# Optimization experiments

Hardware: AMD Instinct MI355X
Metric: run time of the kernel (lower is better)

The kernel has to match this reference:

```python
import jax, jax.numpy as jnp
import numpy as np

N = 300000   # number of occupied voxels (sparse tensor rows)
L = 100      # grid side length -> 1e6 cells, occupancy 0.3
C = 32       # channels (channelwise/depthwise conv)
KS = 3       # kernel_size per axis
D = 3        # spatial dimension
R = (KS - 1) // 2


def _build_sparse_structure():
    """Sample N unique voxel coords and build kernel maps (edge lists) like
    MinkowskiEngine's coordinate manager: for each kernel offset, pairs
    (in_idx, out_idx) such that coords[in_idx] == coords[out_idx] + offset."""
    rng = np.random.default_rng(0)
    flat = rng.choice(L ** 3, size=N, replace=False)
    coords = np.stack([flat // (L * L), (flat // L) % L, flat % L], axis=1).astype(np.int32)
    keys = flat.astype(np.int64)
    order = np.argsort(keys)
    sk = keys[order]
    out_ids = np.arange(N, dtype=np.int64)
    in_list, out_list = [], []
    for dx in range(-R, R + 1):
        for dy in range(-R, R + 1):
            for dz in range(-R, R + 1):
                nx = coords[:, 0].astype(np.int64) + dx
                ny = coords[:, 1].astype(np.int64) + dy
                nz = coords[:, 2].astype(np.int64) + dz
                inb = (nx >= 0) & (nx < L) & (ny >= 0) & (ny < L) & (nz >= 0) & (nz < L)
                nk = (nx * L + ny) * L + nz
                pos = np.searchsorted(sk, nk)
                pos_c = np.clip(pos, 0, N - 1)
                ok = inb & (sk[pos_c] == nk)
                in_list.append(order[pos_c[ok]])
                out_list.append(out_ids[ok])
    in_idx = np.concatenate(in_list).astype(np.int32)
    out_idx = np.concatenate(out_list).astype(np.int32)
    return coords, in_idx, out_idx


def setup_inputs() -> dict:
    coords, in_idx, out_idx = _build_sparse_structure()
    key = jax.random.key(0)
    k1, k2 = jax.random.split(key)
    in_feats = jax.random.normal(k1, (N, C), dtype=jnp.float32)
    kernel = jax.random.normal(k2, (KS ** D, C), dtype=jnp.float32)  # depthwise kernel
    return {
        "coords": jnp.asarray(coords),
        "in_idx": jnp.asarray(in_idx),
        "out_idx": jnp.asarray(out_idx),
        "in_feats": in_feats,
        "kernel": kernel,
    }


def reference(coords, in_idx, out_idx, in_feats, kernel):
    # index_array = KS ** flip(arange(D)) -> [9, 3, 1] for KS=3, D=3
    index_pow = jnp.array([KS ** (D - 1 - i) for i in range(D)], dtype=jnp.int32)
    # tensor_stride = 1; kernel_coord = (C_in - C_out)//1 + (KS-1)//2, per edge [E, D]
    kernel_coord = coords[in_idx] - coords[out_idx] + R
    k1d = jnp.sum(index_pow[None, :] * kernel_coord, axis=1)  # [E] in [0, KS**D)
    # gather-multiply-scatter: out_F[out] += in_feats[in] * kernel[k1d]
    out_F = jnp.zeros_like(in_feats).at[out_idx].add(in_feats[in_idx] * kernel[k1d])
    return out_F
```

## Files before the change

### kernel.cpp

```cpp
#include <hip/hip_runtime.h>

#define NCH 32
#define GROUPS 8
#define KVOL 27
#define LG 100
#define LP 102
#define RGN 5
#define NRGN 20
#define NREGIONS (NRGN * NRGN * NRGN)
#define BSIDE 7
#define BVOL 343
#define CELLS 125
#define LSTR 29

__global__ void build_dense(const int* __restrict__ coords,
                            int* __restrict__ dense, int N) {
    int i = blockIdx.x * blockDim.x + threadIdx.x;
    if (i >= N) return;
    int x = coords[3 * i + 0];
    int y = coords[3 * i + 1];
    int z = coords[3 * i + 2];
    dense[((size_t)(x + 1) * LP + (y + 1)) * LP + (z + 1)] = i + 1;
}

__global__ __launch_bounds__(256) void gather_conv_region(
        const int* __restrict__ dense,
        const float4* __restrict__ in_feats4,
        const float4* __restrict__ kernel4,
        float4* __restrict__ out4) {
    __shared__ float4 kw[(KVOL + 1) * GROUPS];
    __shared__ int brick[BVOL];
    __shared__ int rows[CELLS];
    __shared__ int cnts[CELLS];
    __shared__ int list[CELLS * LSTR];
    __shared__ int cnt;

    int tid = threadIdx.x;

    int b = blockIdx.x;
    const int per = NREGIONS >> 3;
    int r = (b & 7) * per + (b >> 3);

    if (tid == 0) cnt = 0;
    for (int i = tid; i < (KVOL + 1) * GROUPS; i += 256)
        kw[i] = (i < KVOL * GROUPS) ? kernel4[i]
                                    : make_float4(0.f, 0.f, 0.f, 0.f);

    int bx = r / (NRGN * NRGN);
    int by = (r / NRGN) % NRGN;
    int bz = r % NRGN;
    int ox = bx * RGN, oy = by * RGN, oz = bz * RGN;

    for (int i = tid; i < BVOL; i += 256) {
        int lx = i / (BSIDE * BSIDE), ly = (i / BSIDE) % BSIDE, lz = i % BSIDE;
        brick[i] = dense[((size_t)(ox + lx) * LP + (oy + ly)) * LP + (oz + lz)];
    }
    __syncthreads();

    if (tid < CELLS) {
        int cx = tid / (RGN * RGN), cy = (tid / RGN) % RGN, cz = tid % RGN;
        int bidx = (cx + 1) * (BSIDE * BSIDE) + (cy + 1) * BSIDE + (cz + 1);
        int v = brick[bidx];
        if (v > 0) {
            int p = atomicAdd(&cnt, 1);
            int myrow = v - 1;
            rows[p] = myrow;
            int j = 0;
            #pragma unroll
            for (int k = 0; k < KVOL; ++k) {
                int dx = k / 9 - 1, dy = (k / 3) % 3 - 1, dz = k % 3 - 1;
                int nb = brick[bidx + dx * (BSIDE * BSIDE) + dy * BSIDE + dz];
                if (nb > 0) list[p * LSTR + (j++)] = ((nb - 1) << 5) | k;
            }
            while (j & 3) list[p * LSTR + (j++)] = (myrow << 5) | KVOL;
            cnts[p] = j;
        }
    }
    __syncthreads();

    int n  = cnt;
    int lr = tid >> 3;
    int g  = tid & 7;
    for (int base = 0; base < n; base += 32) {
        int lo = base + lr;
        if (lo < n) {
            int cr = cnts[lo];
            const int* tl = &list[lo * LSTR];
            float4 acc = make_float4(0.f, 0.f, 0.f, 0.f);
            for (int j = 0; j < cr; j += 4) {
                int e0 = tl[j + 0], e1 = tl[j + 1];
                int e2 = tl[j + 2], e3 = tl[j + 3];
                float4 f0 = in_feats4[(size_t)(e0 >> 5) * GROUPS + g];
                float4 f1 = in_feats4[(size_t)(e1 >> 5) * GROUPS + g];
                float4 f2 = in_feats4[(size_t)(e2 >> 5) * GROUPS + g];
                float4 f3 = in_feats4[(size_t)(e3 >> 5) * GROUPS + g];
                float4 w0 = kw[(e0 & 31) * GROUPS + g];
                float4 w1 = kw[(e1 & 31) * GROUPS + g];
                float4 w2 = kw[(e2 & 31) * GROUPS + g];
                float4 w3 = kw[(e3 & 31) * GROUPS + g];
                acc.x += f0.x * w0.x; acc.y += f0.y * w0.y;
                acc.z += f0.z * w0.z; acc.w += f0.w * w0.w;
                acc.x += f1.x * w1.x; acc.y += f1.y * w1.y;
                acc.z += f1.z * w1.z; acc.w += f1.w * w1.w;
                acc.x += f2.x * w2.x; acc.y += f2.y * w2.y;
                acc.z += f2.z * w2.z; acc.w += f2.w * w2.w;
                acc.x += f3.x * w3.x; acc.y += f3.y * w3.y;
                acc.z += f3.z * w3.z; acc.w += f3.w * w3.w;
            }
            out4[(size_t)rows[lo] * GROUPS + g] = acc;
        }
    }
}

__global__ void mink_conv_scatter(const int* __restrict__ coords,
                                  const int* __restrict__ in_idx,
                                  const int* __restrict__ out_idx,
                                  const float4* __restrict__ in_feats4,
                                  const float4* __restrict__ kernel4,
                                  float* __restrict__ out,
                                  int E) {
    __shared__ float4 kw[KVOL * GROUPS];
    for (int i = threadIdx.x; i < KVOL * GROUPS; i += blockDim.x)
        kw[i] = kernel4[i];
    __syncthreads();
    int t = blockIdx.x * blockDim.x + threadIdx.x;
    if (t >= E * GROUPS) return;
    int e = t >> 3, g = t & 7;
    int vi = in_idx[e], vo = out_idx[e];
    int c0 = coords[vi * 3 + 0] - coords[vo * 3 + 0] + 1;
    int c1 = coords[vi * 3 + 1] - coords[vo * 3 + 1] + 1;
    int c2 = coords[vi * 3 + 2] - coords[vo * 3 + 2] + 1;
    int k1d = (c0 * 3 + c1) * 3 + c2;
    float4 f = in_feats4[vi * GROUPS + g];
    float4 w = kw[k1d * GROUPS + g];
    float* o = out + vo * NCH + g * 4;
    atomicAdd(o + 0, f.x * w.x);
    atomicAdd(o + 1, f.y * w.y);
    atomicAdd(o + 2, f.z * w.z);
    atomicAdd(o + 3, f.w * w.w);
}

extern "C" void kernel_launch(void* const* d_in, const int* in_sizes, int n_in,
                              void* d_out, int out_size, void* d_ws, size_t ws_size,
                              hipStream_t stream) {
    const int*   coords   = (const int*)d_in[0];
    const int*   in_idx   = (const int*)d_in[1];
    const int*   out_idx  = (const int*)d_in[2];
    const float* in_feats = (const float*)d_in[3];
    const float* kernel   = (const float*)d_in[4];

    const int E     = in_sizes[1];
    const int Nrows = out_size / NCH;

    const size_t dense_bytes = (size_t)LP * LP * LP * sizeof(int);

    if (ws_size >= dense_bytes) {
        int* dense = (int*)d_ws;
        hipMemsetAsync(dense, 0, dense_bytes, stream);

        int block = 256;
        int grid1 = (Nrows + block - 1) / block;
        build_dense<<<grid1, block, 0, stream>>>(coords, dense, Nrows);

        gather_conv_region<<<NREGIONS, 256, 0, stream>>>(
            dense, (const float4*)in_feats, (const float4*)kernel,
            (float4*)d_out);
    } else {
        hipMemsetAsync(d_out, 0, (size_t)out_size * sizeof(float), stream);
        int total = E * GROUPS;
        int block = 256;
        int grid  = (total + block - 1) / block;
        mink_conv_scatter<<<grid, block, 0, stream>>>(
            coords, in_idx, out_idx,
            (const float4*)in_feats, (const float4*)kernel,
            (float*)d_out, E);
    }
}
```

Measured before the change: 144.6 us.

## Stage brick neighbor features in LDS and pack edge lists as 16-bit slot indices

Each region block now assigns LDS slots to all occupied voxels of its 7x7x7 brick, halo included, and loads their features into shared memory once. Edge lists then hold 16-bit slot|offset codes instead of global rows. This removes repeated global gathers of the same neighbor feature rows across the 27 offsets. List building runs on 64 threads while the other threads fill the feature staging buffer, and LDS arrays use a padded stride of 9 float4 per row to reduce bank conflicts. If a brick has more than 167 occupied voxels, a fallback path gathers features from global memory. The larger LDS footprint may lower occupancy.

```diff
diff --git a/kernel.cpp b/kernel.cpp
--- a/kernel.cpp
+++ b/kernel.cpp
@@ -11,7 +11,10 @@
 #define BSIDE 7
 #define BVOL 343
 #define CELLS 125
-#define LSTR 29
+#define FSTRIDE 9
+#define FEAT_SLOTS 168
+#define FEAT_CAP (FEAT_SLOTS - 1)
+#define LSTR 28
 
 __global__ void build_dense(const int* __restrict__ coords,
                             int* __restrict__ dense, int N) {
@@ -28,23 +31,28 @@
         const float4* __restrict__ in_feats4,
         const float4* __restrict__ kernel4,
         float4* __restrict__ out4) {
-    __shared__ float4 kw[(KVOL + 1) * GROUPS];
-    __shared__ int brick[BVOL];
-    __shared__ int rows[CELLS];
-    __shared__ int cnts[CELLS];
-    __shared__ int list[CELLS * LSTR];
-    __shared__ int cnt;
+    __shared__ float4 feat[FEAT_SLOTS * FSTRIDE];
+    __shared__ float4 kw[(KVOL + 1) * FSTRIDE];
+    __shared__ int bs[BVOL];
+    __shared__ int slotrow[BVOL + 1];
+    __shared__ int cellq[CELLS];
+    __shared__ __align__(16) unsigned short list[CELLS * LSTR];
+    __shared__ int nslots, nint;
 
     int tid = threadIdx.x;
+    int g   = tid & 7;
+
+    if (tid == 0) { nslots = 0; nint = 0; slotrow[0] = 0; }
+    if (tid < (KVOL + 1) * GROUPS) {
+        int kr = tid >> 3;
+        kw[kr * FSTRIDE + g] = (kr < KVOL) ? kernel4[kr * GROUPS + g]
+                                           : make_float4(0.f, 0.f, 0.f, 0.f);
+    }
+    if (tid < GROUPS) feat[tid] = make_float4(0.f, 0.f, 0.f, 0.f);
 
     int b = blockIdx.x;
     const int per = NREGIONS >> 3;
     int r = (b & 7) * per + (b >> 3);
-
-    if (tid == 0) cnt = 0;
-    for (int i = tid; i < (KVOL + 1) * GROUPS; i += 256)
-        kw[i] = (i < KVOL * GROUPS) ? kernel4[i]
-                                    : make_float4(0.f, 0.f, 0.f, 0.f);
 
     int bx = r / (NRGN * NRGN);
     int by = (r / NRGN) % NRGN;
@@ -53,61 +61,113 @@
 
     for (int i = tid; i < BVOL; i += 256) {
         int lx = i / (BSIDE * BSIDE), ly = (i / BSIDE) % BSIDE, lz = i % BSIDE;
-        brick[i] = dense[((size_t)(ox + lx) * LP + (oy + ly)) * LP + (oz + lz)];
-    }
-    __syncthreads();
-
-    if (tid < CELLS) {
-        int cx = tid / (RGN * RGN), cy = (tid / RGN) % RGN, cz = tid % RGN;
-        int bidx = (cx + 1) * (BSIDE * BSIDE) + (cy + 1) * BSIDE + (cz + 1);
-        int v = brick[bidx];
+        bs[i] = dense[((size_t)(ox + lx) * LP + (oy + ly)) * LP + (oz + lz)];
+    }
+    __syncthreads();
+
+    for (int i = tid; i < BVOL; i += 256) {
+        int v = bs[i];
+        int s = 0;
         if (v > 0) {
-            int p = atomicAdd(&cnt, 1);
-            int myrow = v - 1;
-            rows[p] = myrow;
+            s = 1 + atomicAdd(&nslots, 1);
+            slotrow[s] = v - 1;
+            int lx = i / 49, ly = (i / 7) % 7, lz = i % 7;
+            if ((unsigned)(lx - 1) < RGN && (unsigned)(ly - 1) < RGN &&
+                (unsigned)(lz - 1) < RGN) {
+                int q = atomicAdd(&nint, 1);
+                cellq[q] = i;
+            }
+        }
+        bs[i] = s;
+    }
+    __syncthreads();
+
+    int ns = nslots;
+    int n  = nint;
+    bool ovf = (ns > FEAT_CAP);
+
+    if (tid < 64) {
+        for (int q = tid; q < n; q += 64) {
+            int bidx = cellq[q];
+            unsigned short* tl = &list[q * LSTR];
             int j = 0;
             #pragma unroll
             for (int k = 0; k < KVOL; ++k) {
                 int dx = k / 9 - 1, dy = (k / 3) % 3 - 1, dz = k % 3 - 1;
-                int nb = brick[bidx + dx * (BSIDE * BSIDE) + dy * BSIDE + dz];
-                if (nb > 0) list[p * LSTR + (j++)] = ((nb - 1) << 5) | k;
-            }
-            while (j & 3) list[p * LSTR + (j++)] = (myrow << 5) | KVOL;
-            cnts[p] = j;
-        }
-    }
-    __syncthreads();
-
-    int n  = cnt;
+                int s = bs[bidx + dx * (BSIDE * BSIDE) + dy * BSIDE + dz];
+                if (s) tl[j++] = (unsigned short)((s << 5) | k);
+            }
+            while (j & 3) tl[j++] = (unsigned short)KVOL;
+            cellq[q] = bidx | (j << 10);
+        }
+    } else {
+        int t   = tid - 64;
+        int lim = ovf ? FEAT_CAP : ns;
+        for (int s = 1 + (t >> 3); s <= lim; s += 24)
+            feat[s * FSTRIDE + g] = in_feats4[slotrow[s] * GROUPS + g];
+    }
+    __syncthreads();
+
     int lr = tid >> 3;
-    int g  = tid & 7;
-    for (int base = 0; base < n; base += 32) {
-        int lo = base + lr;
-        if (lo < n) {
-            int cr = cnts[lo];
-            const int* tl = &list[lo * LSTR];
-            float4 acc = make_float4(0.f, 0.f, 0.f, 0.f);
-            for (int j = 0; j < cr; j += 4) {
-                int e0 = tl[j + 0], e1 = tl[j + 1];
-                int e2 = tl[j + 2], e3 = tl[j + 3];
-                float4 f0 = in_feats4[(size_t)(e0 >> 5) * GROUPS + g];
-                float4 f1 = in_feats4[(size_t)(e1 >> 5) * GROUPS + g];
-                float4 f2 = in_feats4[(size_t)(e2 >> 5) * GROUPS + g];
-                float4 f3 = in_feats4[(size_t)(e3 >> 5) * GROUPS + g];
-                float4 w0 = kw[(e0 & 31) * GROUPS + g];
-                float4 w1 = kw[(e1 & 31) * GROUPS + g];
-                float4 w2 = kw[(e2 & 31) * GROUPS + g];
-                float4 w3 = kw[(e3 & 31) * GROUPS + g];
-                acc.x += f0.x * w0.x; acc.y += f0.y * w0.y;
-                acc.z += f0.z * w0.z; acc.w += f0.w * w0.w;
-                acc.x += f1.x * w1.x; acc.y += f1.y * w1.y;
-                acc.z += f1.z * w1.z; acc.w += f1.w * w1.w;
-                acc.x += f2.x * w2.x; acc.y += f2.y * w2.y;
-                acc.z += f2.z * w2.z; acc.w += f2.w * w2.w;
-                acc.x += f3.x * w3.x; acc.y += f3.y * w3.y;
-                acc.z += f3.z * w3.z; acc.w += f3.w * w3.w;
-            }
-            out4[(size_t)rows[lo] * GROUPS + g] = acc;
+    if (!ovf) {
+        for (int base = 0; base < n; base += 32) {
+            int q = base + lr;
+            if (q < n) {
+                int cq   = cellq[q];
+                int bidx = cq & 1023;
+                int cr   = cq >> 10;
+                int orow = slotrow[bs[bidx]];
+                const uint2* tl2 = (const uint2*)&list[q * LSTR];
+                float4 acc = make_float4(0.f, 0.f, 0.f, 0.f);
+                for (int j = 0; j < cr; j += 4) {
+                    uint2 L = tl2[j >> 2];
+                    int e0 = L.x & 0xffff, e1 = L.x >> 16;
+                    int e2 = L.y & 0xffff, e3 = L.y >> 16;
+                    float4 f0 = feat[(e0 >> 5) * FSTRIDE + g];
+                    float4 w0 = kw[(e0 & 31) * FSTRIDE + g];
+                    float4 f1 = feat[(e1 >> 5) * FSTRIDE + g];
+                    float4 w1 = kw[(e1 & 31) * FSTRIDE + g];
+                    float4 f2 = feat[(e2 >> 5) * FSTRIDE + g];
+                    float4 w2 = kw[(e2 & 31) * FSTRIDE + g];
+                    float4 f3 = feat[(e3 >> 5) * FSTRIDE + g];
+                    float4 w3 = kw[(e3 & 31) * FSTRIDE + g];
+                    acc.x += f0.x * w0.x; acc.y += f0.y * w0.y;
+                    acc.z += f0.z * w0.z; acc.w += f0.w * w0.w;
+                    acc.x += f1.x * w1.x; acc.y += f1.y * w1.y;
+                    acc.z += f1.z * w1.z; acc.w += f1.w * w1.w;
+                    acc.x += f2.x * w2.x; acc.y += f2.y * w2.y;
+                    acc.z += f2.z * w2.z; acc.w += f2.w * w2.w;
+                    acc.x += f3.x * w3.x; acc.y += f3.y * w3.y;
+                    acc.z += f3.z * w3.z; acc.w += f3.w * w3.w;
+                }
+                out4[(size_t)orow * GROUPS + g] = acc;
+            }
+        }
+    } else {
+        for (int base = 0; base < n; base += 32) {
+            int q = base + lr;
+            if (q < n) {
+                int cq   = cellq[q];
+                int bidx = cq & 1023;
+                int cr   = cq >> 10;
+                int orow = slotrow[bs[bidx]];
+                const uint2* tl2 = (const uint2*)&list[q * LSTR];
+                float4 acc = make_float4(0.f, 0.f, 0.f, 0.f);
+                for (int j = 0; j < cr; j += 4) {
+                    uint2 L = tl2[j >> 2];
+                    int ee[4] = { (int)(L.x & 0xffff), (int)(L.x >> 16),
+                                  (int)(L.y & 0xffff), (int)(L.y >> 16) };
+                    #pragma unroll
+                    for (int t = 0; t < 4; ++t) {
+                        int e = ee[t];
+                        float4 f = in_feats4[(size_t)slotrow[e >> 5] * GROUPS + g];
+                        float4 w = kw[(e & 31) * FSTRIDE + g];
+                        acc.x += f.x * w.x; acc.y += f.y * w.y;
+                        acc.z += f.z * w.z; acc.w += f.w * w.w;
+                    }
+                }
+                out4[(size_t)orow * GROUPS + g] = acc;
+            }
         }
     }
 }
@@ -119,9 +179,9 @@
                                   const float4* __restrict__ kernel4,
                                   float* __restrict__ out,
                                   int E) {
-    __shared__ float4 kw[KVOL * GROUPS];
+    __shared__ float4 kws[KVOL * GROUPS];
     for (int i = threadIdx.x; i < KVOL * GROUPS; i += blockDim.x)
-        kw[i] = kernel4[i];
+        kws[i] = kernel4[i];
     __syncthreads();
     int t = blockIdx.x * blockDim.x + threadIdx.x;
     if (t >= E * GROUPS) return;
@@ -132,7 +192,7 @@
     int c2 = coords[vi * 3 + 2] - coords[vo * 3 + 2] + 1;
     int k1d = (c0 * 3 + c1) * 3 + c2;
     float4 f = in_feats4[vi * GROUPS + g];
-    float4 w = kw[k1d * GROUPS + g];
+    float4 w = kws[k1d * GROUPS + g];
     float* o = out + vo * NCH + g * 4;
     atomicAdd(o + 0, f.x * w.x);
     atomicAdd(o + 1, f.y * w.y);
```

New measurement: 154.2 us. 1.07x slower.

## Parallelize neighbor-list build across threads and sort rows by neighbor count

Applied to the files above, without the earlier changes.

Neighbor-list construction in each region block is now spread over all 256 threads, one neighbor offset per thread, instead of one thread per cell looping over 27 offsets. List entries are compressed to 16-bit slot indices that resolve to rows through a shared slot table. Cells are then sorted by padded neighbor count with a histogram, so the 8-thread groups sharing a wavefront do similar amounts of work. The kernel-weight table gets a padded stride to avoid LDS bank conflicts. These changes add several extra barriers, shared atomics and indirect lookups per block.

```diff
diff --git a/kernel.cpp b/kernel.cpp
--- a/kernel.cpp
+++ b/kernel.cpp
@@ -11,7 +11,8 @@
 #define BSIDE 7
 #define BVOL 343
 #define CELLS 125
-#define LSTR 29
+#define FSTR 9
+#define LSTR 28
 
 __global__ void build_dense(const int* __restrict__ coords,
                             int* __restrict__ dense, int N) {
@@ -28,24 +29,30 @@
         const float4* __restrict__ in_feats4,
         const float4* __restrict__ kernel4,
         float4* __restrict__ out4) {
-    __shared__ float4 kw[(KVOL + 1) * GROUPS];
+    __shared__ float4 kw[(KVOL + 1) * FSTR];
     __shared__ int brick[BVOL];
-    __shared__ int rows[CELLS];
-    __shared__ int cnts[CELLS];
-    __shared__ int list[CELLS * LSTR];
-    __shared__ int cnt;
+    __shared__ int slotrow[BVOL];
+    __shared__ int qcell[CELLS];
+    __shared__ int fillA[CELLS];
+    __shared__ int smap[CELLS];
+    __shared__ int hist[7];
+    __shared__ __align__(8) unsigned short list[CELLS * LSTR];
+    __shared__ int nslots, nint;
 
     int tid = threadIdx.x;
+    int g   = tid & 7;
+
+    if (tid == 0) { nslots = 0; nint = 0; }
+    if (tid < 7) hist[tid] = 0;
+    if (tid < CELLS) fillA[tid] = 0;
+    if (tid < (KVOL + 1) * GROUPS) {
+        int kr = tid >> 3;
+        kw[kr * FSTR + g] = (kr < KVOL) ? kernel4[kr * GROUPS + g]
+                                        : make_float4(0.f, 0.f, 0.f, 0.f);
+    }
 
     int b = blockIdx.x;
-    const int per = NREGIONS >> 3;
-    int r = (b & 7) * per + (b >> 3);
-
-    if (tid == 0) cnt = 0;
-    for (int i = tid; i < (KVOL + 1) * GROUPS; i += 256)
-        kw[i] = (i < KVOL * GROUPS) ? kernel4[i]
-                                    : make_float4(0.f, 0.f, 0.f, 0.f);
-
+    int r = (b & 7) * (NREGIONS >> 3) + (b >> 3);
     int bx = r / (NRGN * NRGN);
     int by = (r / NRGN) % NRGN;
     int bz = r % NRGN;
@@ -53,51 +60,81 @@
 
     for (int i = tid; i < BVOL; i += 256) {
         int lx = i / (BSIDE * BSIDE), ly = (i / BSIDE) % BSIDE, lz = i % BSIDE;
-        brick[i] = dense[((size_t)(ox + lx) * LP + (oy + ly)) * LP + (oz + lz)];
-    }
-    __syncthreads();
-
-    if (tid < CELLS) {
-        int cx = tid / (RGN * RGN), cy = (tid / RGN) % RGN, cz = tid % RGN;
-        int bidx = (cx + 1) * (BSIDE * BSIDE) + (cy + 1) * BSIDE + (cz + 1);
-        int v = brick[bidx];
+        int v = dense[((size_t)(ox + lx) * LP + (oy + ly)) * LP + (oz + lz)];
+        int s = 0;
         if (v > 0) {
-            int p = atomicAdd(&cnt, 1);
-            int myrow = v - 1;
-            rows[p] = myrow;
-            int j = 0;
-            #pragma unroll
-            for (int k = 0; k < KVOL; ++k) {
-                int dx = k / 9 - 1, dy = (k / 3) % 3 - 1, dz = k % 3 - 1;
-                int nb = brick[bidx + dx * (BSIDE * BSIDE) + dy * BSIDE + dz];
-                if (nb > 0) list[p * LSTR + (j++)] = ((nb - 1) << 5) | k;
+            s = atomicAdd(&nslots, 1);
+            slotrow[s] = v - 1;
+            if ((unsigned)(lx - 1) < RGN && (unsigned)(ly - 1) < RGN &&
+                (unsigned)(lz - 1) < RGN) {
+                int p = atomicAdd(&nint, 1);
+                qcell[p] = (s << 16) | i;
             }
-            while (j & 3) list[p * LSTR + (j++)] = (myrow << 5) | KVOL;
-            cnts[p] = j;
+            s += 1;
         }
-    }
-    __syncthreads();
-
-    int n  = cnt;
+        brick[i] = s;
+    }
+    __syncthreads();
+
+    int n = nint;
+
+    for (int idx = tid; idx < n * KVOL; idx += 256) {
+        int p = idx / KVOL;
+        int k = idx - p * KVOL;
+        int cell = qcell[p] & 0xffff;
+        int dx = k / 9 - 1, dy = (k / 3) % 3 - 1, dz = k % 3 - 1;
+        int nb = brick[cell + dx * (BSIDE * BSIDE) + dy * BSIDE + dz];
+        if (nb) {
+            int pos = atomicAdd(&fillA[p], 1);
+            list[p * LSTR + pos] = (unsigned short)(((nb - 1) << 5) | k);
+        }
+    }
+    __syncthreads();
+
+    if (tid < n) {
+        int j = fillA[tid];
+        int s = qcell[tid] >> 16;
+        unsigned short dummy = (unsigned short)((s << 5) | KVOL);
+        while (j & 3) list[tid * LSTR + (j++)] = dummy;
+        int bin = (j >> 2) - 1;
+        int h = atomicAdd(&hist[bin], 1);
+        fillA[tid] = j | (bin << 8) | (h << 16);
+    }
+    __syncthreads();
+
+    if (tid < n) {
+        int f = fillA[tid];
+        int j = f & 255, bin = (f >> 8) & 255, h = f >> 16;
+        int pos = h;
+        for (int bb = bin + 1; bb < 7; ++bb) pos += hist[bb];
+        smap[pos] = (tid << 8) | j;
+    }
+    __syncthreads();
+
     int lr = tid >> 3;
-    int g  = tid & 7;
     for (int base = 0; base < n; base += 32) {
         int lo = base + lr;
         if (lo < n) {
-            int cr = cnts[lo];
-            const int* tl = &list[lo * LSTR];
+            int d  = smap[lo];
+            int p  = d >> 8;
+            int nq = (d & 255) >> 2;
+            int orow = slotrow[qcell[p] >> 16];
+            const uint2* tl2 = (const uint2*)&list[p * LSTR];
             float4 acc = make_float4(0.f, 0.f, 0.f, 0.f);
-            for (int j = 0; j < cr; j += 4) {
-                int e0 = tl[j + 0], e1 = tl[j + 1];
-                int e2 = tl[j + 2], e3 = tl[j + 3];
-                float4 f0 = in_feats4[(size_t)(e0 >> 5) * GROUPS + g];
-                float4 f1 = in_feats4[(size_t)(e1 >> 5) * GROUPS + g];
-                float4 f2 = in_feats4[(size_t)(e2 >> 5) * GROUPS + g];
-                float4 f3 = in_feats4[(size_t)(e3 >> 5) * GROUPS + g];
-                float4 w0 = kw[(e0 & 31) * GROUPS + g];
-                float4 w1 = kw[(e1 & 31) * GROUPS + g];
-                float4 w2 = kw[(e2 & 31) * GROUPS + g];
-                float4 w3 = kw[(e3 & 31) * GROUPS + g];
+            for (int jq = 0; jq < nq; ++jq) {
+                uint2 L = tl2[jq];
+                int e0 = L.x & 0xffff, e1 = L.x >> 16;
+                int e2 = L.y & 0xffff, e3 = L.y >> 16;
+                int r0 = slotrow[e0 >> 5], r1 = slotrow[e1 >> 5];
+                int r2 = slotrow[e2 >> 5], r3 = slotrow[e3 >> 5];
+                float4 f0 = in_feats4[(size_t)r0 * GROUPS + g];
+                float4 f1 = in_feats4[(size_t)r1 * GROUPS + g];
+                float4 f2 = in_feats4[(size_t)r2 * GROUPS + g];
+                float4 f3 = in_feats4[(size_t)r3 * GROUPS + g];
+                float4 w0 = kw[(e0 & 31) * FSTR + g];
+                float4 w1 = kw[(e1 & 31) * FSTR + g];
+                float4 w2 = kw[(e2 & 31) * FSTR + g];
+                float4 w3 = kw[(e3 & 31) * FSTR + g];
                 acc.x += f0.x * w0.x; acc.y += f0.y * w0.y;
                 acc.z += f0.z * w0.z; acc.w += f0.w * w0.w;
                 acc.x += f1.x * w1.x; acc.y += f1.y * w1.y;
@@ -107,7 +144,7 @@
                 acc.x += f3.x * w3.x; acc.y += f3.y * w3.y;
                 acc.z += f3.z * w3.z; acc.w += f3.w * w3.w;
             }
-            out4[(size_t)rows[lo] * GROUPS + g] = acc;
+            out4[(size_t)orow * GROUPS + g] = acc;
         }
     }
 }
@@ -119,9 +156,9 @@
                                   const float4* __restrict__ kernel4,
                                   float* __restrict__ out,
                                   int E) {
-    __shared__ float4 kw[KVOL * GROUPS];
+    __shared__ float4 kws[KVOL * GROUPS];
     for (int i = threadIdx.x; i < KVOL * GROUPS; i += blockDim.x)
-        kw[i] = kernel4[i];
+        kws[i] = kernel4[i];
     __syncthreads();
     int t = blockIdx.x * blockDim.x + threadIdx.x;
     if (t >= E * GROUPS) return;
@@ -132,7 +169,7 @@
     int c2 = coords[vi * 3 + 2] - coords[vo * 3 + 2] + 1;
     int k1d = (c0 * 3 + c1) * 3 + c2;
     float4 f = in_feats4[vi * GROUPS + g];
-    float4 w = kw[k1d * GROUPS + g];
+    float4 w = kws[k1d * GROUPS + g];
     float* o = out + vo * NCH + g * 4;
     atomicAdd(o + 0, f.x * w.x);
     atomicAdd(o + 1, f.y * w.y);
```

Result: faster. 139.0 us (-3.9%).
